# Optimization experiments

Hardware: AMD Instinct MI355X
Metric: run time of the kernel (lower is better)

## Reference

```python
import jax, jax.numpy as jnp
import numpy as np

K = 2            # top-k experts
SCALING = 16.0 / 16.0  # alpha / r


def setup_inputs() -> dict:
    key = jax.random.key(0)
    ks = jax.random.split(key, 7)
    B, T, D, O, E, R = 2, 4096, 2048, 2048, 8, 16
    return {
        "x": jax.random.normal(ks[0], (B, T, D), dtype=jnp.float32),
        "W": jax.random.normal(ks[1], (O, D), dtype=jnp.float32) * (1.0 / np.sqrt(D)),
        "b": jax.random.normal(ks[2], (O,), dtype=jnp.float32) * 0.02,
        "lora_A": jax.random.normal(ks[3], (E, R, D), dtype=jnp.float32) * (1.0 / np.sqrt(D)),
        "lora_B": jax.random.normal(ks[4], (E, O, R), dtype=jnp.float32) * 0.02,
        "gate_w": jax.random.normal(ks[5], (E, D), dtype=jnp.float32) * 0.02,
        "gate_b": jax.random.normal(ks[6], (E,), dtype=jnp.float32) * 0.02,
    }


def reference(x, W, b, lora_A, lora_B, gate_w, gate_b):
    orig_shape = x.shape
    D = orig_shape[-1]
    O = W.shape[0]
    x_flat = x.reshape(-1, D)                                  # [N, D]

    base = x_flat @ W.T + b                                    # [N, O]

    logits = x_flat @ gate_w.T + gate_b                        # [N, E] (eval: no noise)
    topk_logits, topk_idx = jax.lax.top_k(logits, K)           # [N, K]
    gates = jax.nn.softmax(topk_logits, axis=-1)               # [N, K]

    xA = jnp.einsum('nd,erd->ner', x_flat, lora_A)             # [N, E, R]
    delta_all = jnp.einsum('ner,eor->neo', xA, lora_B)         # [N, E, O]

    delta_topk = jnp.take_along_axis(delta_all, topk_idx[:, :, None], axis=1)  # [N, K, O]
    lora_update = jnp.sum(delta_topk * gates[:, :, None], axis=1)              # [N, O]

    out = base + SCALING * lora_update
    return out.reshape(*orig_shape[:-1], O)
```

## Files before the change

kernel.cpp:

```cpp
#include <hip/hip_runtime.h>
#include <hip/hip_bf16.h>
#include <stdint.h>

#define N_ROWS 8192
#define DIM    2048
#define OUTD   2048
#define NEXP   8
#define RNK    16
#define ZCOLS  128
#define KAUG   2176

typedef unsigned short u16;
typedef float  f32x4  __attribute__((ext_vector_type(4)));
typedef __bf16 bf16x8 __attribute__((ext_vector_type(8)));

__device__ __forceinline__ u16 f2bf(float f) {
  unsigned u = __float_as_uint(f);
  return (u16)((u + 0x7fffu + ((u >> 16) & 1u)) >> 16);
}

#define GLOAD(SRC, DST) __builtin_amdgcn_global_load_lds( \
    (__attribute__((address_space(1))) void*)(SRC), \
    (__attribute__((address_space(3))) void*)(DST), 16, 0, 0)

__global__ __launch_bounds__(256) void k2_weights(
    const float* __restrict__ W, const float* __restrict__ lB,
    const float* __restrict__ lA, u16* __restrict__ waug, u16* __restrict__ ab)
{
  const int t = threadIdx.x;
  const int bid = blockIdx.x;
  if (bid < OUTD) {
    const int o = bid;
    const float* wr = W + (size_t)o * DIM;
    u16* dst = waug + (size_t)o * KAUG;
    #pragma unroll
    for (int i = 0; i < 2; ++i) {
      int c = t * 4 + i * 1024;
      float4 v = *(const float4*)(wr + c);
      ushort4 s; s.x = f2bf(v.x); s.y = f2bf(v.y); s.z = f2bf(v.z); s.w = f2bf(v.w);
      *(ushort4*)(dst + c) = s;
    }
    if (t < ZCOLS) {
      int e = t >> 4, r = t & 15;
      dst[DIM + t] = f2bf(lB[((size_t)e * OUTD + o) * RNK + r]);
    }
  } else {
    const int ar = bid - OUTD;
    const float* src = lA + (size_t)ar * DIM;
    u16* dst = ab + (size_t)ar * DIM;
    #pragma unroll
    for (int i = 0; i < 2; ++i) {
      int c = t * 4 + i * 1024;
      float4 v = *(const float4*)(src + c);
      ushort4 s; s.x = f2bf(v.x); s.y = f2bf(v.y); s.z = f2bf(v.z); s.w = f2bf(v.w);
      *(ushort4*)(dst + c) = s;
    }
  }
}

__global__ __launch_bounds__(256) void kf_fused(
    const float* __restrict__ x, const float* __restrict__ gw,
    const float* __restrict__ gb, const u16* __restrict__ ab,
    u16* __restrict__ xaug)
{
  __shared__ __align__(16) u16 la[2][8192];
  __shared__ __align__(16) u16 xb[1024];
  __shared__ float4 gates[16];

  const int t    = threadIdx.x;
  const int wave = t >> 6;
  const int lane = t & 63;
  const int r    = t >> 4;
  const int q    = t & 15;
  const size_t row0 = (size_t)blockIdx.x * 16;

  int   lrow[4], lsch[4];
  #pragma unroll
  for (int i = 0; i < 4; ++i) {
    const int g = t + i * 256;
    lrow[i] = g >> 3;
    lsch[i] = (g & 7) ^ (lrow[i] & 7);
  }

  auto stage_la = [&](int c, int h) {
    const int C0 = c * 64;
    #pragma unroll
    for (int i = 0; i < 4; ++i) {
      const char* src = (const char*)(ab + (size_t)lrow[i] * DIM + C0 + lsch[i] * 8);
      GLOAD(src, (char*)la[h] + (wave * 64 + i * 256) * 16);
    }
  };

  float4 xv, gwv[8];
  xv = *(const float4*)(x + (row0 + r) * DIM + q * 4);
  #pragma unroll
  for (int e = 0; e < NEXP; ++e)
    gwv[e] = *(const float4*)(gw + (size_t)e * DIM + q * 4);

  stage_la(0, 0);
  __builtin_amdgcn_sched_barrier(0);

  float ga[NEXP] = {};
  f32x4 acc[2] = {};
  const int nfA = 2 * wave, nfB = 2 * wave + 1;

  for (int c = 0; c < 32; ++c) {
    const int C0 = c * 64;
    if (c + 1 < 32) stage_la(c + 1, (c + 1) & 1);
    __builtin_amdgcn_sched_barrier(0);
    float4 xvn, gwvn[8];
    if (c + 1 < 32) {
      xvn = *(const float4*)(x + (row0 + r) * DIM + C0 + 64 + q * 4);
      #pragma unroll
      for (int e = 0; e < NEXP; ++e)
        gwvn[e] = *(const float4*)(gw + (size_t)e * DIM + C0 + 64 + q * 4);
    }
    __builtin_amdgcn_sched_barrier(0);
    ushort4 s; s.x = f2bf(xv.x); s.y = f2bf(xv.y); s.z = f2bf(xv.z); s.w = f2bf(xv.w);
    *(ushort4*)(xaug + (row0 + r) * KAUG + C0 + q * 4) = s;
    #pragma unroll
    for (int e = 0; e < NEXP; ++e)
      ga[e] += xv.x * gwv[e].x + xv.y * gwv[e].y + xv.z * gwv[e].z + xv.w * gwv[e].w;
    {
      const int ch = q >> 1;
      const int by = r * 128 + ((ch ^ (r & 7)) * 16) + (q & 1) * 8;
      *(ushort4*)((char*)xb + by) = s;
    }
    asm volatile("s_waitcnt vmcnt(0) lgkmcnt(0)" ::: "memory");
    __builtin_amdgcn_sched_barrier(0);
    __builtin_amdgcn_s_barrier();

    const char* lab = (const char*)la[c & 1];
    #pragma unroll
    for (int ks = 0; ks < 2; ++ks) {
      const int ra  = lane & 15;
      const int pa  = ((ks * 4 + (lane >> 4)) ^ (ra & 7)) * 16;
      bf16x8 avf = *(const bf16x8*)((char*)xb + ra * 128 + pa);
      const int rbA = (lane & 15) + 16 * nfA;
      const int rbB = (lane & 15) + 16 * nfB;
      bf16x8 bvA = *(const bf16x8*)(lab + rbA * 128 + (((ks * 4 + (lane >> 4)) ^ (rbA & 7)) * 16));
      bf16x8 bvB = *(const bf16x8*)(lab + rbB * 128 + (((ks * 4 + (lane >> 4)) ^ (rbB & 7)) * 16));
      acc[0] = __builtin_amdgcn_mfma_f32_16x16x32_bf16(avf, bvA, acc[0], 0, 0, 0);
      acc[1] = __builtin_amdgcn_mfma_f32_16x16x32_bf16(avf, bvB, acc[1], 0, 0, 0);
    }
    __builtin_amdgcn_s_barrier();
    __builtin_amdgcn_sched_barrier(0);
    xv = xvn;
    #pragma unroll
    for (int e = 0; e < NEXP; ++e) gwv[e] = gwvn[e];
  }

  #pragma unroll
  for (int e = 0; e < NEXP; ++e) {
    float v = ga[e];
    v += __shfl_xor(v, 1); v += __shfl_xor(v, 2);
    v += __shfl_xor(v, 4); v += __shfl_xor(v, 8);
    ga[e] = v + gb[e];
  }
  if (q == 0) {
    int e0 = 0; float m0 = ga[0];
    #pragma unroll
    for (int e = 1; e < NEXP; ++e) if (ga[e] > m0) { m0 = ga[e]; e0 = e; }
    int e1 = (e0 == 0) ? 1 : 0; float m1 = ga[e1];
    #pragma unroll
    for (int e = 0; e < NEXP; ++e) if (e != e0 && ga[e] > m1) { m1 = ga[e]; e1 = e; }
    float tt  = expf(m1 - m0);
    float inv = 1.f / (1.f + tt);
    float4 gg; gg.x = inv; gg.y = tt * inv;
    gg.z = __int_as_float(e0); gg.w = __int_as_float(e1);
    gates[r] = gg;
  }
  __syncthreads();

  #pragma unroll
  for (int nfl = 0; nfl < 2; ++nfl) {
    const int e = 2 * wave + nfl;
    const int n = e * 16 + (lane & 15);
    #pragma unroll
    for (int j = 0; j < 4; ++j) {
      const int m = (lane >> 4) * 4 + j;
      float4 gg = gates[m];
      const float g = (e == __float_as_int(gg.z)) ? gg.x
                    : ((e == __float_as_int(gg.w)) ? gg.y : 0.f);
      xaug[(row0 + m) * KAUG + DIM + n] = f2bf(acc[nfl][j] * g);
    }
  }
}

#define LGKM0 do { asm volatile("s_waitcnt lgkmcnt(0)" ::: "memory"); \
                   __builtin_amdgcn_sched_barrier(0); } while (0)
#define PH_END do { __builtin_amdgcn_s_barrier(); \
                    __builtin_amdgcn_sched_barrier(0); } while (0)
#define MFMA_G(AV, BV, NFB) do { \
  __builtin_amdgcn_s_setprio(1); \
  _Pragma("unroll") \
  for (int mf = 0; mf < 8; ++mf) { \
    acc[mf][NFB]     = __builtin_amdgcn_mfma_f32_16x16x32_bf16(AV[mf], BV[NFB],     acc[mf][NFB],     0, 0, 0); \
    acc[mf][NFB + 1] = __builtin_amdgcn_mfma_f32_16x16x32_bf16(AV[mf], BV[NFB + 1], acc[mf][NFB + 1], 0, 0, 0); \
  } \
  __builtin_amdgcn_s_setprio(0); \
} while (0)
#define RD_A(DST, BASE, XOR) do { _Pragma("unroll") \
  for (int mf = 0; mf < 8; ++mf) \
    DST[mf] = *(const bf16x8*)((BASE) + ((offA0) ^ (XOR)) + mf * 2048); } while (0)
#define RD_B(DST, BASE, XOR) do { _Pragma("unroll") \
  for (int nf = 0; nf < 4; ++nf) \
    DST[nf] = *(const bf16x8*)((BASE) + ((offB0) ^ (XOR)) + nf * 2048); } while (0)

__global__ __launch_bounds__(512, 2) void gemm256_pipe(
    const u16* __restrict__ A, int lda,
    const u16* __restrict__ Bm, int ldb,
    int Ksz, int grid_n,
    float* __restrict__ outF, int ldo, const float* __restrict__ bias)
{
  __shared__ __align__(16) u16 smem[65536];

  const int tid  = threadIdx.x;
  const int wave = tid >> 6;
  const int lane = tid & 63;

  int bid = blockIdx.x;
  const int nwg = gridDim.x;
  if ((nwg & 7) == 0) {
    const int cpx = nwg >> 3;
    bid = (bid & 7) * cpx + (bid >> 3);
  }
  const int tm = bid / grid_n;
  const int tn = bid % grid_n;
  const size_t row0 = (size_t)tm * 256;
  const size_t col0 = (size_t)tn * 256;

  const int l3  = lane >> 3;
  const int sch = ((lane & 7) ^ l3) << 4;
  const char* aSrc = (const char*)(A  + (row0 + (size_t)(wave * 8 + l3)) * lda) + sch;
  const char* bSrc = (const char*)(Bm + (col0 + (size_t)(wave * 8 + l3)) * ldb) + sch;
  const size_t arst = (size_t)lda * 128;
  const size_t brst = (size_t)ldb * 128;
  char* ldsA = (char*)smem + wave * 1024;
  char* ldsB = (char*)smem + 65536 + wave * 1024;

  auto stageA = [&](int tt) {
    const size_t ko = (size_t)tt * 128;
    const int    sb = (tt & 1) << 15;
    #pragma unroll
    for (int i = 0; i < 4; ++i)
      GLOAD(aSrc + ko + i * arst, ldsA + sb + i * 8192);
  };
  auto stageB = [&](int tt) {
    const size_t ko = (size_t)tt * 128;
    const int    sb = (tt & 1) << 15;
    #pragma unroll
    for (int i = 0; i < 4; ++i)
      GLOAD(bSrc + ko + i * brst, ldsB + sb + i * 8192);
  };

  const int wm = wave >> 2, wn = wave & 3;
  const int x0 = ((lane >> 4) ^ (lane & 7)) << 4;
  const int offA0 = wm * 16384 + (lane & 15) * 128 + x0;
  const int offB0 = wn * 8192  + (lane & 15) * 128 + x0;

  f32x4 acc[8][4] = {};

  const int nk    = Ksz / 64;
  const int niter = nk / 2;

  stageA(0); stageB(0); stageA(1); stageB(1);
  asm volatile("s_waitcnt vmcnt(8)" ::: "memory");
  __builtin_amdgcn_s_barrier();
  __builtin_amdgcn_sched_barrier(0);

  for (int it = 0; it < niter; ++it) {
    const int T = 2 * it;
    const bool more = (it + 1 < niter);
    const char* sa0 = (const char*)smem;
    const char* sb0 = (const char*)smem + 65536;
    const char* sa1 = (const char*)smem + 32768;
    const char* sb1 = (const char*)smem + 98304;
    bf16x8 av0[8], bv0[4], av1[8], bv1[4];

    RD_A(av0, sa0, 0); RD_B(bv0, sb0, 0);
    __builtin_amdgcn_s_barrier(); LGKM0;
    MFMA_G(av0, bv0, 0); PH_END;
    RD_A(av1, sa0, 64);
    __builtin_amdgcn_s_barrier(); LGKM0;
    MFMA_G(av0, bv0, 2); PH_END;
    RD_B(bv1, sb0, 64);
    if (more) stageA(T + 2);
    __builtin_amdgcn_s_barrier(); LGKM0;
    MFMA_G(av1, bv1, 0); PH_END;
    if (more) asm volatile("s_waitcnt vmcnt(4)" ::: "memory");
    else      asm volatile("s_waitcnt vmcnt(0)" ::: "memory");
    __builtin_amdgcn_sched_barrier(0);
    if (more) stageB(T + 2);
    __builtin_amdgcn_s_barrier();
    __builtin_amdgcn_sched_barrier(0);
    MFMA_G(av1, bv1, 2); PH_END;
    RD_A(av0, sa1, 0); RD_B(bv0, sb1, 0);
    __builtin_amdgcn_s_barrier(); LGKM0;
    MFMA_G(av0, bv0, 0); PH_END;
    RD_A(av1, sa1, 64);
    __builtin_amdgcn_s_barrier(); LGKM0;
    MFMA_G(av0, bv0, 2); PH_END;
    RD_B(bv1, sb1, 64);
    if (more) stageA(T + 3);
    __builtin_amdgcn_s_barrier(); LGKM0;
    MFMA_G(av1, bv1, 0); PH_END;
    if (more) asm volatile("s_waitcnt vmcnt(4)" ::: "memory");
    else      asm volatile("s_waitcnt vmcnt(0)" ::: "memory");
    __builtin_amdgcn_sched_barrier(0);
    if (more) stageB(T + 3);
    __builtin_amdgcn_s_barrier();
    __builtin_amdgcn_sched_barrier(0);
    MFMA_G(av1, bv1, 2); PH_END;
  }

  #pragma unroll
  for (int nf = 0; nf < 4; ++nf) {
    const size_t c = col0 + wn * 64 + nf * 16 + (lane & 15);
    const float bvv = bias[c];
    #pragma unroll
    for (int mf = 0; mf < 8; ++mf) {
      const size_t rb = row0 + wm * 128 + mf * 16 + ((lane >> 4) << 2);
      #pragma unroll
      for (int j = 0; j < 4; ++j)
        outF[(rb + j) * (size_t)ldo + c] = acc[mf][nf][j] + bvv;
    }
  }
}

extern "C" void kernel_launch(void* const* d_in, const int* in_sizes, int n_in,
                              void* d_out, int out_size, void* d_ws, size_t ws_size,
                              hipStream_t stream) {
  const float* x  = (const float*)d_in[0];
  const float* W  = (const float*)d_in[1];
  const float* b  = (const float*)d_in[2];
  const float* lA = (const float*)d_in[3];
  const float* lB = (const float*)d_in[4];
  const float* gw = (const float*)d_in[5];
  const float* gb = (const float*)d_in[6];
  float* out = (float*)d_out;

  u16* xaug = (u16*)d_ws;
  u16* waug = xaug + (size_t)N_ROWS * KAUG;
  u16* ab   = waug + (size_t)OUTD * KAUG;

  hipLaunchKernelGGL(k2_weights, dim3(OUTD + ZCOLS), dim3(256), 0, stream,
                     W, lB, lA, waug, ab);
  hipLaunchKernelGGL(kf_fused, dim3(N_ROWS / 16), dim3(256), 0, stream,
                     x, gw, gb, ab, xaug);
  hipLaunchKernelGGL(gemm256_pipe,
                     dim3((N_ROWS / 256) * (OUTD / 256)), dim3(512), 0, stream,
                     xaug, KAUG, waug, KAUG, KAUG, OUTD / 256,
                     out, OUTD, b);
}
```

Measured before the change: 126.8 us.

## Restructure GEMM main loop into quadrant phases with split half-tile staging

Rewrites the 256x256 GEMM main loop to process one K-tile per iteration in four quadrant phases. Each A and B tile is staged in two halves interleaved with the MFMA phases, and B is prefetched two tiles ahead, to overlap global-to-LDS loads with compute more finely. It also changes the LDS read pattern and the register set (single av array, two bv halves). The pre-GEMM kernel now issues its LDS staging before the register loads and uses a relaxed vmcnt wait so the next chunk's loads stay in flight. The finer scheduling adds barriers and relies on exact vmcnt counts, which could stall or be miscounted.

```diff
diff --git a/kernel.cpp b/kernel.cpp
--- a/kernel.cpp
+++ b/kernel.cpp
@@ -91,14 +91,14 @@
     }
   };
 
+  stage_la(0, 0);
+  __builtin_amdgcn_sched_barrier(0);
+
   float4 xv, gwv[8];
   xv = *(const float4*)(x + (row0 + r) * DIM + q * 4);
   #pragma unroll
   for (int e = 0; e < NEXP; ++e)
     gwv[e] = *(const float4*)(gw + (size_t)e * DIM + q * 4);
-
-  stage_la(0, 0);
-  __builtin_amdgcn_sched_barrier(0);
 
   float ga[NEXP] = {};
   f32x4 acc[2] = {};
@@ -126,7 +126,8 @@
       const int by = r * 128 + ((ch ^ (r & 7)) * 16) + (q & 1) * 8;
       *(ushort4*)((char*)xb + by) = s;
     }
-    asm volatile("s_waitcnt vmcnt(0) lgkmcnt(0)" ::: "memory");
+    if (c + 1 < 32) asm volatile("s_waitcnt vmcnt(22) lgkmcnt(0)" ::: "memory");
+    else            asm volatile("s_waitcnt vmcnt(0) lgkmcnt(0)" ::: "memory");
     __builtin_amdgcn_sched_barrier(0);
     __builtin_amdgcn_s_barrier();
 
@@ -189,23 +190,29 @@
 
 #define LGKM0 do { asm volatile("s_waitcnt lgkmcnt(0)" ::: "memory"); \
                    __builtin_amdgcn_sched_barrier(0); } while (0)
-#define PH_END do { __builtin_amdgcn_s_barrier(); \
-                    __builtin_amdgcn_sched_barrier(0); } while (0)
-#define MFMA_G(AV, BV, NFB) do { \
+#define MFMA_Q(MH, NH) do { \
   __builtin_amdgcn_s_setprio(1); \
   _Pragma("unroll") \
-  for (int mf = 0; mf < 8; ++mf) { \
-    acc[mf][NFB]     = __builtin_amdgcn_mfma_f32_16x16x32_bf16(AV[mf], BV[NFB],     acc[mf][NFB],     0, 0, 0); \
-    acc[mf][NFB + 1] = __builtin_amdgcn_mfma_f32_16x16x32_bf16(AV[mf], BV[NFB + 1], acc[mf][NFB + 1], 0, 0, 0); \
-  } \
+  for (int mf4 = 0; mf4 < 4; ++mf4) \
+    _Pragma("unroll") \
+    for (int nfq = 0; nfq < 2; ++nfq) { \
+      acc[(MH)*4+mf4][(NH)*2+nfq] = __builtin_amdgcn_mfma_f32_16x16x32_bf16( \
+          av[mf4*2+0], bv##NH[nfq*2+0], acc[(MH)*4+mf4][(NH)*2+nfq], 0, 0, 0); \
+      acc[(MH)*4+mf4][(NH)*2+nfq] = __builtin_amdgcn_mfma_f32_16x16x32_bf16( \
+          av[mf4*2+1], bv##NH[nfq*2+1], acc[(MH)*4+mf4][(NH)*2+nfq], 0, 0, 0); \
+    } \
   __builtin_amdgcn_s_setprio(0); \
 } while (0)
-#define RD_A(DST, BASE, XOR) do { _Pragma("unroll") \
-  for (int mf = 0; mf < 8; ++mf) \
-    DST[mf] = *(const bf16x8*)((BASE) + ((offA0) ^ (XOR)) + mf * 2048); } while (0)
-#define RD_B(DST, BASE, XOR) do { _Pragma("unroll") \
-  for (int nf = 0; nf < 4; ++nf) \
-    DST[nf] = *(const bf16x8*)((BASE) + ((offB0) ^ (XOR)) + nf * 2048); } while (0)
+#define RD_AH(SA, MH) do { _Pragma("unroll") \
+  for (int i = 0; i < 8; ++i) { \
+    const int mf = (MH)*4 + (i >> 1); \
+    av[i] = *(const bf16x8*)((SA) + mf * 2048 + aRow + (xK ^ ((i & 1) << 6))); \
+  } } while (0)
+#define RD_B2(DST, SB, NH) do { _Pragma("unroll") \
+  for (int j = 0; j < 4; ++j) { \
+    const int nf = (NH)*2 + (j >> 1); \
+    DST[j] = *(const bf16x8*)((SB) + bRow + nf * 2048 + (xK ^ ((j & 1) << 6))); \
+  } } while (0)
 
 __global__ __launch_bounds__(512, 2) void gemm256_pipe(
     const u16* __restrict__ A, int lda,
@@ -239,88 +246,71 @@
   char* ldsA = (char*)smem + wave * 1024;
   char* ldsB = (char*)smem + 65536 + wave * 1024;
 
-  auto stageA = [&](int tt) {
+  auto stageA = [&](int tt, int h) {
     const size_t ko = (size_t)tt * 128;
-    const int    sb = (tt & 1) << 15;
-    #pragma unroll
-    for (int i = 0; i < 4; ++i)
-      GLOAD(aSrc + ko + i * arst, ldsA + sb + i * 8192);
+    const int    db = (tt & 1) * 32768 + h * 16384;
+    GLOAD(aSrc + ko + (2 * h + 0) * arst, ldsA + db);
+    GLOAD(aSrc + ko + (2 * h + 1) * arst, ldsA + db + 8192);
   };
-  auto stageB = [&](int tt) {
+  auto stageB = [&](int tt, int h) {
     const size_t ko = (size_t)tt * 128;
-    const int    sb = (tt & 1) << 15;
-    #pragma unroll
-    for (int i = 0; i < 4; ++i)
-      GLOAD(bSrc + ko + i * brst, ldsB + sb + i * 8192);
+    const int    db = (tt & 1) * 32768 + h * 16384;
+    GLOAD(bSrc + ko + (2 * h + 0) * brst, ldsB + db);
+    GLOAD(bSrc + ko + (2 * h + 1) * brst, ldsB + db + 8192);
   };
 
   const int wm = wave >> 2, wn = wave & 3;
-  const int x0 = ((lane >> 4) ^ (lane & 7)) << 4;
-  const int offA0 = wm * 16384 + (lane & 15) * 128 + x0;
-  const int offB0 = wn * 8192  + (lane & 15) * 128 + x0;
+  const int l15 = lane & 15, l16 = lane >> 4;
+  const int aRow = l15 * 128;
+  const int bRow = ((wn & 1) * 64 + l15) * 128;
+  const int xK   = ((l16 ^ (l15 & 7)) << 4);
 
   f32x4 acc[8][4] = {};
-
-  const int nk    = Ksz / 64;
-  const int niter = nk / 2;
-
-  stageA(0); stageB(0); stageA(1); stageB(1);
-  asm volatile("s_waitcnt vmcnt(8)" ::: "memory");
-  __builtin_amdgcn_s_barrier();
-  __builtin_amdgcn_sched_barrier(0);
-
-  for (int it = 0; it < niter; ++it) {
-    const int T = 2 * it;
-    const bool more = (it + 1 < niter);
-    const char* sa0 = (const char*)smem;
-    const char* sb0 = (const char*)smem + 65536;
-    const char* sa1 = (const char*)smem + 32768;
-    const char* sb1 = (const char*)smem + 98304;
-    bf16x8 av0[8], bv0[4], av1[8], bv1[4];
-
-    RD_A(av0, sa0, 0); RD_B(bv0, sb0, 0);
+  bf16x8 av[8], bv0[4], bv1[4];
+
+  const int nk = Ksz / 64;
+
+  stageA(0, 0); stageA(0, 1); stageB(0, 0); stageB(0, 1);
+  stageB(1, 0); stageB(1, 1);
+
+  for (int t = 0; t < nk; ++t) {
+    const char* sa = (const char*)smem + (t & 1) * 32768 + wm * 16384;
+    const char* sb = (const char*)smem + 65536 + (t & 1) * 32768 + (wn >> 1) * 16384;
+
+    if (t + 1 < nk) asm volatile("s_waitcnt vmcnt(4)" ::: "memory");
+    else            asm volatile("s_waitcnt vmcnt(0)" ::: "memory");
+    __builtin_amdgcn_sched_barrier(0);
+    __builtin_amdgcn_s_barrier();
+
+    RD_AH(sa, 0); RD_B2(bv0, sb, 0);
+    if (t + 1 < nk) stageA(t + 1, 0);
     __builtin_amdgcn_s_barrier(); LGKM0;
-    MFMA_G(av0, bv0, 0); PH_END;
-    RD_A(av1, sa0, 64);
+    MFMA_Q(0, 0);
+    __builtin_amdgcn_s_barrier();
+
+    RD_B2(bv1, sb, 1);
+    if (t + 1 < nk) stageA(t + 1, 1);
     __builtin_amdgcn_s_barrier(); LGKM0;
-    MFMA_G(av0, bv0, 2); PH_END;
-    RD_B(bv1, sb0, 64);
-    if (more) stageA(T + 2);
+    MFMA_Q(0, 1);
+    __builtin_amdgcn_s_barrier();
+
+    RD_AH(sa, 1);
+    if (t + 2 < nk) stageB(t + 2, 0);
     __builtin_amdgcn_s_barrier(); LGKM0;
-    MFMA_G(av1, bv1, 0); PH_END;
-    if (more) asm volatile("s_waitcnt vmcnt(4)" ::: "memory");
-    else      asm volatile("s_waitcnt vmcnt(0)" ::: "memory");
-    __builtin_amdgcn_sched_barrier(0);
-    if (more) stageB(T + 2);
-    __builtin_amdgcn_s_barrier();
-    __builtin_amdgcn_sched_barrier(0);
-    MFMA_G(av1, bv1, 2); PH_END;
-    RD_A(av0, sa1, 0); RD_B(bv0, sb1, 0);
-    __builtin_amdgcn_s_barrier(); LGKM0;
-    MFMA_G(av0, bv0, 0); PH_END;
-    RD_A(av1, sa1, 64);
-    __builtin_amdgcn_s_barrier(); LGKM0;
-    MFMA_G(av0, bv0, 2); PH_END;
-    RD_B(bv1, sb1, 64);
-    if (more) stageA(T + 3);
-    __builtin_amdgcn_s_barrier(); LGKM0;
-    MFMA_G(av1, bv1, 0); PH_END;
-    if (more) asm volatile("s_waitcnt vmcnt(4)" ::: "memory");
-    else      asm volatile("s_waitcnt vmcnt(0)" ::: "memory");
-    __builtin_amdgcn_sched_barrier(0);
-    if (more) stageB(T + 3);
-    __builtin_amdgcn_s_barrier();
-    __builtin_amdgcn_sched_barrier(0);
-    MFMA_G(av1, bv1, 2); PH_END;
+    MFMA_Q(1, 1);
+    __builtin_amdgcn_s_barrier();
+
+    if (t + 2 < nk) stageB(t + 2, 1);
+    MFMA_Q(1, 0);
   }
 
   #pragma unroll
   for (int nf = 0; nf < 4; ++nf) {
-    const size_t c = col0 + wn * 64 + nf * 16 + (lane & 15);
+    const size_t c = col0 + wn * 64 + nf * 16 + l15;
     const float bvv = bias[c];
     #pragma unroll
     for (int mf = 0; mf < 8; ++mf) {
-      const size_t rb = row0 + wm * 128 + mf * 16 + ((lane >> 4) << 2);
+      const size_t rb = row0 + wm * 128 + mf * 16 + (l16 << 2);
       #pragma unroll
       for (int j = 0; j < 4; ++j)
         outF[(rb + j) * (size_t)ldo + c] = acc[mf][nf][j] + bvv;
```

New measurement: 121.9 us. 1.04x faster.
